# Optimization experiments

Hardware: AMD Instinct MI355X
Metric: run time of the kernel (lower is better)

Reference implementation:

```python
import jax, jax.numpy as jnp
import numpy as np
from jax import lax

DN = ('NCHW', 'OIHW', 'NCHW')

def _edge_bank():
    # All eight fixed stencils embedded in 5x5 (3x3 kernels zero-padded to center),
    # equivalent to the original per-kernel SAME conv. Order matches torch.cat order:
    # sobel_x, sobel_y, diag1, diag2, laplacian, gradient5x5, scharr_x, scharr_y
    k3 = [
        [[-1, 0, 1], [-2, 0, 2], [-1, 0, 1]],            # sobel_x
        [[-1, -2, -1], [0, 0, 0], [1, 2, 1]],            # sobel_y
        [[0, 1, 2], [-1, 0, 1], [-2, -1, 0]],            # diag1
        [[-2, -1, 0], [-1, 0, 1], [0, 1, 2]],            # diag2
        [[0, 1, 0], [1, -4, 1], [0, 1, 0]],              # laplacian
    ]
    g5 = [[-1, -2, 0, 2, 1], [-2, -3, 0, 3, 2], [-3, -4, 0, 4, 3],
          [-2, -3, 0, 3, 2], [-1, -2, 0, 2, 1]]          # gradient5x5
    s3 = [
        [[-3, 0, 3], [-10, 0, 10], [-3, 0, 3]],          # scharr_x
        [[-3, -10, -3], [0, 0, 0], [3, 10, 3]],          # scharr_y
    ]
    ks = []
    for k in k3:
        ks.append(np.pad(np.asarray(k, np.float32), 1))
    ks.append(np.asarray(g5, np.float32))
    for k in s3:
        ks.append(np.pad(np.asarray(k, np.float32), 1))
    return jnp.asarray(np.stack(ks)[:, None, :, :])  # [8,1,5,5]

EDGE_BANK = _edge_bank()

def _conv(x, w, p):
    return lax.conv_general_dilated(x, w, (1, 1), [(p, p), (p, p)], dimension_numbers=DN)

def setup_inputs() -> dict:
    key = jax.random.key(0)
    k = jax.random.split(key, 7)
    x  = jax.random.normal(k[0], (8, 1, 512, 512), jnp.float32)
    w1 = jax.random.normal(k[1], (32, 9, 3, 3), jnp.float32) * 0.05
    b1 = jax.random.normal(k[2], (32,), jnp.float32) * 0.01
    w2 = jax.random.normal(k[3], (16, 32, 3, 3), jnp.float32) * 0.05
    b2 = jax.random.normal(k[4], (16,), jnp.float32) * 0.01
    wr = jax.random.normal(k[5], (16, 1, 1, 1), jnp.float32) * 0.05
    br = jax.random.normal(k[6], (16,), jnp.float32) * 0.01
    return {"x": x, "w1": w1, "b1": b1, "w2": w2, "b2": b2, "wr": wr, "br": br}

def reference(x, w1, b1, w2, b2, wr, br):
    grads = _conv(x, EDGE_BANK, 2)                         # [B,8,H,W] all stencils in one pass
    feats = jnp.concatenate([grads, x], axis=1)            # [B,9,H,W]
    h = jax.nn.relu(_conv(feats, w1, 1) + b1[None, :, None, None])
    fused = jax.nn.relu(_conv(h, w2, 1) + b2[None, :, None, None])
    residual = _conv(x, wr, 0) + br[None, :, None, None]
    return fused + residual
```

## Files before the change

### kernel.cpp

```cpp
#include <hip/hip_runtime.h>
#include <hip/hip_bf16.h>


typedef __attribute__((ext_vector_type(8))) short bf16x8;
typedef __attribute__((ext_vector_type(4))) float f32x4;

#define XS_S 28

#define WS_A2   5120
#define WS_SB   9728
#define WS_FLT  5120
#define WS_WEFF 12800
#define WS_A2I  14848
#define WS_BYTES 38912

__device__ const float EB[9][5][5] = {
 {{0,0,0,0,0},{0,-1,0,1,0},{0,-2,0,2,0},{0,-1,0,1,0},{0,0,0,0,0}},
 {{0,0,0,0,0},{0,-1,-2,-1,0},{0,0,0,0,0},{0,1,2,1,0},{0,0,0,0,0}},
 {{0,0,0,0,0},{0,0,1,2,0},{0,-1,0,1,0},{0,-2,-1,0,0},{0,0,0,0,0}},
 {{0,0,0,0,0},{0,-2,-1,0,0},{0,-1,0,1,0},{0,0,1,2,0},{0,0,0,0,0}},
 {{0,0,0,0,0},{0,0,1,0,0},{0,1,-4,1,0},{0,0,1,0,0},{0,0,0,0,0}},
 {{-1,-2,0,2,1},{-2,-3,0,3,2},{-3,-4,0,4,3},{-2,-3,0,3,2},{-1,-2,0,2,1}},
 {{0,0,0,0,0},{0,-3,0,3,0},{0,-10,0,10,0},{0,-3,0,3,0},{0,0,0,0,0}},
 {{0,0,0,0,0},{0,-3,-10,-3,0},{0,0,0,0,0},{0,3,10,3,0},{0,0,0,0,0}},
 {{0,0,0,0,0},{0,0,0,0,0},{0,0,1,0,0},{0,0,0,0,0},{0,0,0,0,0}},
};

__device__ __forceinline__ unsigned short f2bf(float f) {
    union { float f; unsigned u; } v; v.f = f;
    unsigned u = v.u + 0x7fffu + ((v.u >> 16) & 1u);
    return (unsigned short)(u >> 16);
}
__device__ __forceinline__ unsigned pk(float lo, float hi) {
    return (unsigned)f2bf(lo) | ((unsigned)f2bf(hi) << 16);
}

__device__ __forceinline__ float weff_tap(const float* __restrict__ w1,
                                          int oc, int dy, int dx) {
    float s = 0.f;
    for (int ch = 0; ch < 9; ++ch)
        for (int ty = 0; ty < 3; ++ty)
            for (int tx = 0; tx < 3; ++tx) {
                int sy = dy - ty, sx = dx - tx;
                if (sy >= 0 && sy < 5 && sx >= 0 && sx < 5)
                    s += w1[(oc * 9 + ch) * 9 + ty * 3 + tx] * EB[ch][sy][sx];
            }
    return s;
}

__global__ __launch_bounds__(256) void setup_frags(
    const float* __restrict__ w1, const float* __restrict__ b1,
    const float* __restrict__ w2, const float* __restrict__ b2,
    const float* __restrict__ wr, const float* __restrict__ br,
    short* __restrict__ ws)
{
    __shared__ float w1s[2592];
    __shared__ float w2s[4608];
    __shared__ float ebs[225];
    const int tid = threadIdx.x;

    for (int i = tid; i < 2592; i += 256) w1s[i] = w1[i];
    for (int i = tid; i < 4608; i += 256) w2s[i] = w2[i];
    if (tid < 225) ebs[tid] = ((const float*)EB)[tid];
    __syncthreads();

    for (int idx = tid; idx < 5120; idx += 256) {
        int i = idx & 7, lane = (idx >> 3) & 63, rest = idx >> 9;
        int mt = rest / 5, ks = rest - 5 * mt;
        int n = lane & 15, lg = lane >> 4;
        int k = 32 * ks + 8 * lg + i;
        int g = k >> 4, ch = k & 15;
        float w = (g < 9 && ch < 9) ? w1s[(mt * 16 + n) * 81 + ch * 9 + g] : 0.f;
        ws[idx] = (short)f2bf(w);
    }
    for (int idx = tid; idx < 4608; idx += 256) {
        int i = idx & 7, lane = (idx >> 3) & 63, ks = idx >> 9;
        int n = lane & 15, lg = lane >> 4;
        int ic = 8 * lg + i;
        ws[WS_A2 + idx] = (short)f2bf(w2s[n * 288 + ic * 9 + ks]);
    }
    for (int idx = tid; idx < 4608; idx += 256) {
        int i = idx & 7, lane = (idx >> 3) & 63, ks = idx >> 9;
        int n = lane & 15, lg = lane >> 4;
        int ic = ((i & 1) << 4) | (lg << 2) | ((i >> 1) & 3);
        ws[WS_A2I + idx] = (short)f2bf(w2s[n * 288 + ic * 9 + ks]);
    }
    for (int idx = tid; idx < 512; idx += 256) {
        int i = idx & 7, lane = idx >> 3;
        int n = lane & 15, lg = lane >> 4;
        int k = 8 * lg + i;
        float v = (k < 25 && n < 9) ? ebs[n * 25 + k] : 0.f;
        ws[WS_SB + idx] = (short)f2bf(v);
    }
    for (int idx = tid; idx < 2048; idx += 256) {
        int i = idx & 7, lane = (idx >> 3) & 63, rest = idx >> 9;
        int mt = rest >> 1, ks = rest & 1;
        int n = lane & 15, lg = lane >> 4;
        int dy = 4 * ks + lg, dx = i;
        float s = 0.f;
        if (dy < 7 && dx < 7) {
            int oc = mt * 16 + n;
            for (int ch = 0; ch < 9; ++ch)
                for (int ty = 0; ty < 3; ++ty) {
                    int sy = dy - ty;
                    if (sy < 0 || sy >= 5) continue;
                    for (int tx = 0; tx < 3; ++tx) {
                        int sx = dx - tx;
                        if (sx >= 0 && sx < 5)
                            s += w1s[(oc * 9 + ch) * 9 + ty * 3 + tx] * ebs[ch * 25 + sy * 5 + sx];
                    }
                }
        }
        ws[WS_WEFF + idx] = (short)f2bf(s);
    }
    if (tid < 64) {
        int lg = tid >> 4;
        float* wf = (float*)ws + WS_FLT + tid * 20;
        for (int r = 0; r < 4; ++r) {
            wf[r]      = b1[lg * 4 + r];
            wf[4 + r]  = b1[16 + lg * 4 + r];
            wf[8 + r]  = b2[lg * 4 + r];
            wf[12 + r] = wr[lg * 4 + r];
            wf[16 + r] = br[lg * 4 + r];
        }
    }
}

template<bool USE_WS>
__global__ __launch_bounds__(256, 4) void edge_interior3(
    const float* __restrict__ x,  const float* __restrict__ w1, const float* __restrict__ b1,
    const float* __restrict__ w2, const float* __restrict__ b2,
    const float* __restrict__ wr, const float* __restrict__ br,
    const short* __restrict__ ws, float* __restrict__ out)
{
    __shared__ long long pool[39168 / 8];
    short* hsS   = (short*)pool;
    float* stage = (float*)pool;

    const int tid  = threadIdx.x;
    const int lane = tid & 63;
    const int wave = tid >> 6;
    const int n    = lane & 15;
    const int lg   = lane >> 4;
    const int bx = blockIdx.x * 32;
    const int by = (blockIdx.y + 1) * 16;
    const int b  = blockIdx.z;
    const float* xb = x + ((size_t)b << 18);

    bf16x8 wa[2][2], a2[9];
    float b1v[2][4], b2v[4], wrv[4], brv[4];
    if (USE_WS) {
#pragma unroll
        for (int mt = 0; mt < 2; ++mt)
#pragma unroll
            for (int ks = 0; ks < 2; ++ks)
                wa[mt][ks] = *reinterpret_cast<const bf16x8*>(
                    &ws[WS_WEFF + ((mt * 2 + ks) * 64 + lane) * 8]);
#pragma unroll
        for (int ks = 0; ks < 9; ++ks)
            a2[ks] = *reinterpret_cast<const bf16x8*>(&ws[WS_A2I + (ks * 64 + lane) * 8]);
        const float* wf = (const float*)ws + WS_FLT + lane * 20;
        f32x4 t0 = *reinterpret_cast<const f32x4*>(wf);
        f32x4 t1 = *reinterpret_cast<const f32x4*>(wf + 4);
        f32x4 t2 = *reinterpret_cast<const f32x4*>(wf + 8);
        f32x4 t3 = *reinterpret_cast<const f32x4*>(wf + 12);
        f32x4 t4 = *reinterpret_cast<const f32x4*>(wf + 16);
#pragma unroll
        for (int r = 0; r < 4; ++r) {
            b1v[0][r] = t0[r]; b1v[1][r] = t1[r];
            b2v[r] = t2[r]; wrv[r] = t3[r]; brv[r] = t4[r];
        }
    } else {
#pragma unroll
        for (int mt = 0; mt < 2; ++mt)
#pragma unroll
            for (int ks = 0; ks < 2; ++ks)
#pragma unroll
                for (int i = 0; i < 8; ++i) {
                    int dy = 4 * ks + lg, dx = i;
                    float s = (dy < 7 && dx < 7) ? weff_tap(w1, mt * 16 + n, dy, dx) : 0.f;
                    wa[mt][ks][i] = (short)f2bf(s);
                }
#pragma unroll
        for (int ks = 0; ks < 9; ++ks)
#pragma unroll
            for (int i = 0; i < 8; ++i) {
                int ic = ((i & 1) << 4) | (lg << 2) | ((i >> 1) & 3);
                a2[ks][i] = (short)f2bf(w2[(n * 32 + ic) * 9 + ks]);
            }
#pragma unroll
        for (int r = 0; r < 4; ++r) {
            b1v[0][r] = b1[lg * 4 + r]; b1v[1][r] = b1[16 + lg * 4 + r];
            b2v[r] = b2[lg * 4 + r]; wrv[r] = wr[lg * 4 + r]; brv[r] = br[lg * 4 + r];
        }
    }

    for (int t = wave; t < 39; t += 4) {
        int p  = t * 16 + n;
        int pc = p < 611 ? p : 611;
        int r1 = pc / 34, c1 = pc - 34 * r1;
        int gxb = bx - 4 + c1; gxb = gxb < 0 ? 0 : (gxb > 504 ? 504 : gxb);
        int gyb = by - 4 + r1;
        f32x4 acc0 = {0.f,0.f,0.f,0.f}, acc1 = {0.f,0.f,0.f,0.f};
#pragma unroll
        for (int ks = 0; ks < 2; ++ks) {
            const int dy = 4 * ks + lg;
            bf16x8 bv = {0,0,0,0,0,0,0,0};
            if (dy < 7) {
                int gy = gyb + dy; gy = gy < 0 ? 0 : (gy > 511 ? 511 : gy);
                const float* xp = xb + ((size_t)gy << 9) + gxb;
                uint4 u;
                u.x = pk(xp[0], xp[1]); u.y = pk(xp[2], xp[3]);
                u.z = pk(xp[4], xp[5]); u.w = pk(xp[6], xp[7]);
                bv = *reinterpret_cast<bf16x8*>(&u);
            }
            acc0 = __builtin_amdgcn_mfma_f32_16x16x32_bf16(wa[0][ks], bv, acc0, 0, 0, 0);
            acc1 = __builtin_amdgcn_mfma_f32_16x16x32_bf16(wa[1][ks], bv, acc1, 0, 0, 0);
        }
        if (p < 612) {
            float h0 = fmaxf(acc0[0] + b1v[0][0], 0.f), g0 = fmaxf(acc1[0] + b1v[1][0], 0.f);
            float h1 = fmaxf(acc0[1] + b1v[0][1], 0.f), g1 = fmaxf(acc1[1] + b1v[1][1], 0.f);
            float h2 = fmaxf(acc0[2] + b1v[0][2], 0.f), g2 = fmaxf(acc1[2] + b1v[1][2], 0.f);
            float h3 = fmaxf(acc0[3] + b1v[0][3], 0.f), g3 = fmaxf(acc1[3] + b1v[1][3], 0.f);
            uint4 W;
            W.x = pk(h0, g0); W.y = pk(h1, g1); W.z = pk(h2, g2); W.w = pk(h3, g3);
            int grp = lg ^ (p & 3);
            *reinterpret_cast<uint4*>(&hsS[p * 32 + grp * 8]) = W;
        }
    }
    __syncthreads();

    const int q0 = wave >> 1;
    const int hh = wave & 1;
    f32x4 oreg[8];
#pragma unroll
    for (int j = 0; j < 2; ++j) {
        const int q = q0 + 2 * j;
        f32x4 acc[4] = {{0.f,0.f,0.f,0.f},{0.f,0.f,0.f,0.f},
                        {0.f,0.f,0.f,0.f},{0.f,0.f,0.f,0.f}};
#pragma unroll
        for (int rr = 0; rr < 6; ++rr) {
#pragma unroll
            for (int dx = 0; dx < 3; ++dx) {
                const int px = (4 * q + rr) * 34 + 16 * hh + n + dx;
                const int grp = lg ^ (px & 3);
                bf16x8 hf = *reinterpret_cast<const bf16x8*>(&hsS[px * 32 + grp * 8]);
#pragma unroll
                for (int o = 0; o < 4; ++o) {
                    const int dy = rr - o;
                    if (dy >= 0 && dy < 3)
                        acc[o] = __builtin_amdgcn_mfma_f32_16x16x32_bf16(
                            a2[dy * 3 + dx], hf, acc[o], 0, 0, 0);
                }
            }
        }
#pragma unroll
        for (int o = 0; o < 4; ++o) {
            const int oy = 4 * q + o;
            float xv = xb[((size_t)(by + oy) << 9) + bx + 16 * hh + n];
            f32x4 ov;
#pragma unroll
            for (int r = 0; r < 4; ++r)
                ov[r] = fmaxf(acc[o][r] + b2v[r], 0.f) + wrv[r] * xv + brv[r];
            oreg[4 * j + o] = ov;
        }
    }
    __syncthreads();

#pragma unroll
    for (int j = 0; j < 2; ++j) {
        const int q = q0 + 2 * j;
#pragma unroll
        for (int o = 0; o < 4; ++o)
#pragma unroll
            for (int r = 0; r < 4; ++r)
                stage[(lg * 4 + r) * 576 + (4 * q + o) * 36 + 16 * hh + n] = oreg[4 * j + o][r];
    }
    __syncthreads();

#pragma unroll
    for (int k = 0; k < 8; ++k) {
        int idx = k * 256 + tid;
        int c   = idx & 7;
        int row = (idx >> 3) & 15;
        int oc  = idx >> 7;
        f32x4 v = *reinterpret_cast<const f32x4*>(&stage[oc * 576 + row * 36 + 4 * c]);
        __builtin_nontemporal_store(v, reinterpret_cast<f32x4*>(
            &out[(((size_t)b * 16 + oc) * 512 + (by + row)) * 512 + bx + 4 * c]));
    }
}

template<bool USE_WS>
__global__ __launch_bounds__(256, 4) void edge_border(
    const float* __restrict__ x,  const float* __restrict__ w1, const float* __restrict__ b1,
    const float* __restrict__ w2, const float* __restrict__ b2,
    const float* __restrict__ wr, const float* __restrict__ br,
    const short* __restrict__ ws, float* __restrict__ out)
{
    __shared__ short fs2[2 * 400 * 8];
    __shared__ short hs4[4 * 324 * 8];
    __shared__ short xs[24 * XS_S];

    const int tid  = threadIdx.x;
    const int lane = tid & 63;
    const int wave = tid >> 6;
    const int n    = lane & 15;
    const int lg   = lane >> 4;

    int idx = blockIdx.x, tx, ty;
    if      (idx < 32) { tx = idx;      ty = 0;  }
    else if (idx < 64) { tx = idx - 32; ty = 31; }
    else if (idx < 94) { tx = 0;        ty = idx - 63; }
    else               { tx = 31;       ty = idx - 93; }
    const int bx = tx * 16, by = ty * 16, b = blockIdx.z;

    for (int i = tid; i < 576; i += 256) {
        int r = i / 24, c = i % 24;
        int gy = by - 4 + r, gx = bx - 4 + c;
        float v = 0.f;
        if (gy >= 0 && gy < 512 && gx >= 0 && gx < 512) v = x[((size_t)b * 512 + gy) * 512 + gx];
        __hip_bfloat16 h = __float2bfloat16(v);
        xs[r * XS_S + c] = *reinterpret_cast<short*>(&h);
    }

    bf16x8 a1[2][5], a2[9], sb;
    float b1v[2][4], b2v[4], wrv[4], brv[4];
    if (USE_WS) {
#pragma unroll
        for (int mt = 0; mt < 2; ++mt)
#pragma unroll
            for (int ks = 0; ks < 5; ++ks)
                a1[mt][ks] = *reinterpret_cast<const bf16x8*>(&ws[((mt * 5 + ks) * 64 + lane) * 8]);
#pragma unroll
        for (int ks = 0; ks < 9; ++ks)
            a2[ks] = *reinterpret_cast<const bf16x8*>(&ws[WS_A2 + (ks * 64 + lane) * 8]);
        sb = *reinterpret_cast<const bf16x8*>(&ws[WS_SB + lane * 8]);
        const float* wf = (const float*)ws + WS_FLT + lane * 20;
        f32x4 t0 = *reinterpret_cast<const f32x4*>(wf);
        f32x4 t1 = *reinterpret_cast<const f32x4*>(wf + 4);
        f32x4 t2 = *reinterpret_cast<const f32x4*>(wf + 8);
        f32x4 t3 = *reinterpret_cast<const f32x4*>(wf + 12);
        f32x4 t4 = *reinterpret_cast<const f32x4*>(wf + 16);
#pragma unroll
        for (int r = 0; r < 4; ++r) {
            b1v[0][r] = t0[r]; b1v[1][r] = t1[r];
            b2v[r] = t2[r]; wrv[r] = t3[r]; brv[r] = t4[r];
        }
    } else {
#pragma unroll
        for (int mt = 0; mt < 2; ++mt)
#pragma unroll
            for (int ks = 0; ks < 5; ++ks)
#pragma unroll
                for (int i = 0; i < 8; ++i) {
                    int k = 32 * ks + 8 * lg + i;
                    int g = k >> 4, ch = k & 15;
                    float w = (g < 9 && ch < 9) ? w1[(mt * 16 + n) * 81 + ch * 9 + g] : 0.f;
                    a1[mt][ks][i] = (short)f2bf(w);
                }
#pragma unroll
        for (int ks = 0; ks < 9; ++ks)
#pragma unroll
            for (int i = 0; i < 8; ++i)
                a2[ks][i] = (short)f2bf(w2[n * 288 + (8 * lg + i) * 9 + ks]);
#pragma unroll
        for (int i = 0; i < 8; ++i) {
            int k = 8 * lg + i;
            float v = (k < 25 && n < 9) ? EB[n][k / 5][k % 5] : 0.f;
            sb[i] = (short)f2bf(v);
        }
#pragma unroll
        for (int r = 0; r < 4; ++r) {
            b1v[0][r] = b1[lg * 4 + r]; b1v[1][r] = b1[16 + lg * 4 + r];
            b2v[r] = b2[lg * 4 + r]; wrv[r] = wr[lg * 4 + r]; brv[r] = br[lg * 4 + r];
        }
    }

    int toff[8];
#pragma unroll
    for (int i = 0; i < 8; ++i) {
        int k = 8 * lg + i;
        int t = k < 25 ? k : 24;
        toff[i] = (t / 5) * XS_S + (t % 5);
    }
    int boff[5];
#pragma unroll
    for (int ks = 0; ks < 5; ++ks) {
        int g = 2 * ks + (lg >> 1); if (g > 8) g = 8;
        int dy = g / 3, dx = g - 3 * dy;
        boff[ks] = (lg & 1) * 3200 + (dy * 20 + dx) * 8;
    }

    __syncthreads();

    for (int t = wave; t < 25; t += 4) {
        int px = t * 16 + n;
        int r = px / 20, c = px - 20 * r;
        const short* base = &xs[r * XS_S + c];
        bf16x8 bv;
#pragma unroll
        for (int i = 0; i < 8; ++i) bv[i] = base[toff[i]];
        f32x4 f = {0.f, 0.f, 0.f, 0.f};
        f = __builtin_amdgcn_mfma_f32_16x16x32_bf16(sb, bv, f, 0, 0, 0);
        int fy = by + r - 2, fx = bx + c - 2;
        float m = (fy >= 0 && fy < 512 && fx >= 0 && fx < 512) ? 1.f : 0.f;
        uint2 wv;
        wv.x = pk(f[0] * m, f[1] * m);
        wv.y = pk(f[2] * m, f[3] * m);
        *reinterpret_cast<uint2*>(&fs2[((lg >> 1) * 400 + px) * 8 + 4 * (lg & 1)]) = wv;
    }
    __syncthreads();

    for (int t = wave; t < 21; t += 4) {
        int p  = t * 16 + n;
        int pc = p < 323 ? p : 323;
        int r1 = pc / 18, c1 = pc - 18 * r1;
        int base = (r1 * 20 + c1) * 8;
        f32x4 acc0 = {0.f,0.f,0.f,0.f}, acc1 = {0.f,0.f,0.f,0.f};
#pragma unroll
        for (int ks = 0; ks < 5; ++ks) {
            bf16x8 bf = *reinterpret_cast<const bf16x8*>(&fs2[base + boff[ks]]);
            acc0 = __builtin_amdgcn_mfma_f32_16x16x32_bf16(a1[0][ks], bf, acc0, 0, 0, 0);
            acc1 = __builtin_amdgcn_mfma_f32_16x16x32_bf16(a1[1][ks], bf, acc1, 0, 0, 0);
        }
        if (p < 324) {
            int hy = by - 1 + r1, hx = bx - 1 + c1;
            float m = (hy >= 0 && hy < 512 && hx >= 0 && hx < 512) ? 1.f : 0.f;
            uint2 W0;
            W0.x = pk(fmaxf(acc0[0] + b1v[0][0], 0.f) * m, fmaxf(acc0[1] + b1v[0][1], 0.f) * m);
            W0.y = pk(fmaxf(acc0[2] + b1v[0][2], 0.f) * m, fmaxf(acc0[3] + b1v[0][3], 0.f) * m);
            *reinterpret_cast<uint2*>(&hs4[((lg >> 1) * 324 + p) * 8 + 4 * (lg & 1)]) = W0;
            uint2 W1;
            W1.x = pk(fmaxf(acc1[0] + b1v[1][0], 0.f) * m, fmaxf(acc1[1] + b1v[1][1], 0.f) * m);
            W1.y = pk(fmaxf(acc1[2] + b1v[1][2], 0.f) * m, fmaxf(acc1[3] + b1v[1][3], 0.f) * m);
            *reinterpret_cast<uint2*>(&hs4[((2 + (lg >> 1)) * 324 + p) * 8 + 4 * (lg & 1)]) = W1;
        }
    }
    __syncthreads();

    const int hbase = lg * 324 * 8;
#pragma unroll
    for (int j = 0; j < 4; ++j) {
        int oy = wave + 4 * j;
        f32x4 acc = {0.f,0.f,0.f,0.f};
#pragma unroll
        for (int ks = 0; ks < 9; ++ks) {
            const int dy = ks / 3, dx = ks - 3 * (ks / 3);
            bf16x8 hf = *reinterpret_cast<const bf16x8*>(
                &hs4[hbase + ((oy + dy) * 18 + n + dx) * 8]);
            acc = __builtin_amdgcn_mfma_f32_16x16x32_bf16(a2[ks], hf, acc, 0, 0, 0);
        }
        __hip_bfloat16 xh = *reinterpret_cast<const __hip_bfloat16*>(&xs[(oy + 4) * XS_S + n + 4]);
        float xv = __bfloat162float(xh);
        float* op = out + (((size_t)(b * 16 + lg * 4) * 512 + (by + oy)) * 512) + bx + n;
#pragma unroll
        for (int r = 0; r < 4; ++r) {
            float o = fmaxf(acc[r] + b2v[r], 0.f) + wrv[r] * xv + brv[r];
            *op = o;
            op += 262144;
        }
    }
}

extern "C" void kernel_launch(void* const* d_in, const int* in_sizes, int n_in,
                              void* d_out, int out_size, void* d_ws, size_t ws_size,
                              hipStream_t stream) {
    const float* x  = (const float*)d_in[0];
    const float* w1 = (const float*)d_in[1];
    const float* b1 = (const float*)d_in[2];
    const float* w2 = (const float*)d_in[3];
    const float* b2 = (const float*)d_in[4];
    const float* wr = (const float*)d_in[5];
    const float* br = (const float*)d_in[6];
    float* out = (float*)d_out;
    short* ws = (short*)d_ws;

    dim3 block(256);
    dim3 gin(16, 30, 8);
    dim3 gbd(124, 1, 8);
    if (ws_size >= WS_BYTES) {
        hipLaunchKernelGGL(setup_frags, dim3(1), dim3(256), 0, stream,
                           w1, b1, w2, b2, wr, br, ws);
        hipLaunchKernelGGL(edge_interior3<true>, gin, block, 0, stream,
                           x, w1, b1, w2, b2, wr, br, ws, out);
        hipLaunchKernelGGL(edge_border<true>, gbd, block, 0, stream,
                           x, w1, b1, w2, b2, wr, br, ws, out);
    } else {
        hipLaunchKernelGGL(edge_interior3<false>, gin, block, 0, stream,
                           x, w1, b1, w2, b2, wr, br, ws, out);
        hipLaunchKernelGGL(edge_border<false>, gbd, block, 0, stream,
                           x, w1, b1, w2, b2, wr, br, ws, out);
    }
}
```

Baseline: 107.9 us.

## Use hardware bf16 pack, stronger LDS swizzle, and drop interior row clamps

Replaces the hand-rolled float-to-bf16 rounding with the __float22bfloat162_rn intrinsic, so packing can use native conversion instructions. Extends the XOR swizzle of the h tile in shared memory with a second term from bits 2-3 of the pixel index, to spread the conv2 fragment reads over more LDS banks. Removes the row clamp on interior global loads, since interior blocks never read outside the image. The risks are small: rounding should match for finite values, but NaN handling may differ.

```diff
diff --git a/kernel.cpp b/kernel.cpp
--- a/kernel.cpp
+++ b/kernel.cpp
@@ -31,8 +31,9 @@
     unsigned u = v.u + 0x7fffu + ((v.u >> 16) & 1u);
     return (unsigned short)(u >> 16);
 }
-__device__ __forceinline__ unsigned pk(float lo, float hi) {
-    return (unsigned)f2bf(lo) | ((unsigned)f2bf(hi) << 16);
+__device__ __forceinline__ unsigned pk2(float lo, float hi) {
+    __hip_bfloat162 h = __float22bfloat162_rn(make_float2(lo, hi));
+    return *reinterpret_cast<unsigned*>(&h);
 }
 
 __device__ __forceinline__ float weff_tap(const float* __restrict__ w1,
@@ -127,7 +128,7 @@
 }
 
 template<bool USE_WS>
-__global__ __launch_bounds__(256, 4) void edge_interior3(
+__global__ __launch_bounds__(256, 4) void edge_interior4(
     const float* __restrict__ x,  const float* __restrict__ w1, const float* __restrict__ b1,
     const float* __restrict__ w2, const float* __restrict__ b2,
     const float* __restrict__ wr, const float* __restrict__ br,
@@ -200,18 +201,17 @@
         int pc = p < 611 ? p : 611;
         int r1 = pc / 34, c1 = pc - 34 * r1;
         int gxb = bx - 4 + c1; gxb = gxb < 0 ? 0 : (gxb > 504 ? 504 : gxb);
-        int gyb = by - 4 + r1;
+        const int gyb = by - 4 + r1;
         f32x4 acc0 = {0.f,0.f,0.f,0.f}, acc1 = {0.f,0.f,0.f,0.f};
 #pragma unroll
         for (int ks = 0; ks < 2; ++ks) {
             const int dy = 4 * ks + lg;
             bf16x8 bv = {0,0,0,0,0,0,0,0};
             if (dy < 7) {
-                int gy = gyb + dy; gy = gy < 0 ? 0 : (gy > 511 ? 511 : gy);
-                const float* xp = xb + ((size_t)gy << 9) + gxb;
+                const float* xp = xb + ((size_t)(gyb + dy) << 9) + gxb;
                 uint4 u;
-                u.x = pk(xp[0], xp[1]); u.y = pk(xp[2], xp[3]);
-                u.z = pk(xp[4], xp[5]); u.w = pk(xp[6], xp[7]);
+                u.x = pk2(xp[0], xp[1]); u.y = pk2(xp[2], xp[3]);
+                u.z = pk2(xp[4], xp[5]); u.w = pk2(xp[6], xp[7]);
                 bv = *reinterpret_cast<bf16x8*>(&u);
             }
             acc0 = __builtin_amdgcn_mfma_f32_16x16x32_bf16(wa[0][ks], bv, acc0, 0, 0, 0);
@@ -223,8 +223,8 @@
             float h2 = fmaxf(acc0[2] + b1v[0][2], 0.f), g2 = fmaxf(acc1[2] + b1v[1][2], 0.f);
             float h3 = fmaxf(acc0[3] + b1v[0][3], 0.f), g3 = fmaxf(acc1[3] + b1v[1][3], 0.f);
             uint4 W;
-            W.x = pk(h0, g0); W.y = pk(h1, g1); W.z = pk(h2, g2); W.w = pk(h3, g3);
-            int grp = lg ^ (p & 3);
+            W.x = pk2(h0, g0); W.y = pk2(h1, g1); W.z = pk2(h2, g2); W.w = pk2(h3, g3);
+            const int grp = lg ^ (p & 3) ^ ((p >> 2) & 3);
             *reinterpret_cast<uint4*>(&hsS[p * 32 + grp * 8]) = W;
         }
     }
@@ -240,10 +240,11 @@
                         {0.f,0.f,0.f,0.f},{0.f,0.f,0.f,0.f}};
 #pragma unroll
         for (int rr = 0; rr < 6; ++rr) {
+            const int pxb = (4 * q + rr) * 34 + 16 * hh + n;
 #pragma unroll
             for (int dx = 0; dx < 3; ++dx) {
-                const int px = (4 * q + rr) * 34 + 16 * hh + n + dx;
-                const int grp = lg ^ (px & 3);
+                const int px = pxb + dx;
+                const int grp = lg ^ (px & 3) ^ ((px >> 2) & 3);
                 bf16x8 hf = *reinterpret_cast<const bf16x8*>(&hsS[px * 32 + grp * 8]);
 #pragma unroll
                 for (int o = 0; o < 4; ++o) {
@@ -405,8 +406,8 @@
         int fy = by + r - 2, fx = bx + c - 2;
         float m = (fy >= 0 && fy < 512 && fx >= 0 && fx < 512) ? 1.f : 0.f;
         uint2 wv;
-        wv.x = pk(f[0] * m, f[1] * m);
-        wv.y = pk(f[2] * m, f[3] * m);
+        wv.x = pk2(f[0] * m, f[1] * m);
+        wv.y = pk2(f[2] * m, f[3] * m);
         *reinterpret_cast<uint2*>(&fs2[((lg >> 1) * 400 + px) * 8 + 4 * (lg & 1)]) = wv;
     }
     __syncthreads();
@@ -427,12 +428,12 @@
             int hy = by - 1 + r1, hx = bx - 1 + c1;
             float m = (hy >= 0 && hy < 512 && hx >= 0 && hx < 512) ? 1.f : 0.f;
             uint2 W0;
-            W0.x = pk(fmaxf(acc0[0] + b1v[0][0], 0.f) * m, fmaxf(acc0[1] + b1v[0][1], 0.f) * m);
-            W0.y = pk(fmaxf(acc0[2] + b1v[0][2], 0.f) * m, fmaxf(acc0[3] + b1v[0][3], 0.f) * m);
+            W0.x = pk2(fmaxf(acc0[0] + b1v[0][0], 0.f) * m, fmaxf(acc0[1] + b1v[0][1], 0.f) * m);
+            W0.y = pk2(fmaxf(acc0[2] + b1v[0][2], 0.f) * m, fmaxf(acc0[3] + b1v[0][3], 0.f) * m);
             *reinterpret_cast<uint2*>(&hs4[((lg >> 1) * 324 + p) * 8 + 4 * (lg & 1)]) = W0;
             uint2 W1;
-            W1.x = pk(fmaxf(acc1[0] + b1v[1][0], 0.f) * m, fmaxf(acc1[1] + b1v[1][1], 0.f) * m);
-            W1.y = pk(fmaxf(acc1[2] + b1v[1][2], 0.f) * m, fmaxf(acc1[3] + b1v[1][3], 0.f) * m);
+            W1.x = pk2(fmaxf(acc1[0] + b1v[1][0], 0.f) * m, fmaxf(acc1[1] + b1v[1][1], 0.f) * m);
+            W1.y = pk2(fmaxf(acc1[2] + b1v[1][2], 0.f) * m, fmaxf(acc1[3] + b1v[1][3], 0.f) * m);
             *reinterpret_cast<uint2*>(&hs4[((2 + (lg >> 1)) * 324 + p) * 8 + 4 * (lg & 1)]) = W1;
         }
     }
@@ -481,12 +482,12 @@
     if (ws_size >= WS_BYTES) {
         hipLaunchKernelGGL(setup_frags, dim3(1), dim3(256), 0, stream,
                            w1, b1, w2, b2, wr, br, ws);
-        hipLaunchKernelGGL(edge_interior3<true>, gin, block, 0, stream,
+        hipLaunchKernelGGL(edge_interior4<true>, gin, block, 0, stream,
                            x, w1, b1, w2, b2, wr, br, ws, out);
         hipLaunchKernelGGL(edge_border<true>, gbd, block, 0, stream,
                            x, w1, b1, w2, b2, wr, br, ws, out);
     } else {
-        hipLaunchKernelGGL(edge_interior3<false>, gin, block, 0, stream,
+        hipLaunchKernelGGL(edge_interior4<false>, gin, block, 0, stream,
                            x, w1, b1, w2, b2, wr, br, ws, out);
         hipLaunchKernelGGL(edge_border<false>, gbd, block, 0, stream,
                            x, w1, b1, w2, b2, wr, br, ws, out);
```

After: 106.5 us. No clear change (-1.2%).
